# Kernel optimization log

Hardware: AMD Instinct MI355X
Metric: run time of the kernel (lower is better)

Reference implementation:

```python
import jax, jax.numpy as jnp
import numpy as np

N_ROW = 50000
N_COL = 50000
E = 600000
D = 128
NEG_SLOPE = 0.01  # torch LeakyReLU default


def _leaky(x):
    return jnp.where(x >= 0, x, NEG_SLOPE * x)


def _mlp(x, W1, b1, W2, b2):
    # (Linear -> LeakyReLU) x2, matching nn.Sequential in Conv_layer
    h = _leaky(x @ W1 + b1)
    return _leaky(h @ W2 + b2)


def setup_inputs() -> dict:
    key = jax.random.key(0)
    ks = jax.random.split(key, 16)
    inp = {
        "feat_row": jax.random.normal(ks[0], (N_ROW, D), jnp.float32),
        "feat_col": jax.random.normal(ks[1], (N_COL, D), jnp.float32),
        "src_c2r": jax.random.randint(ks[2], (E,), 0, N_COL, jnp.int32),
        "dst_c2r": jax.random.randint(ks[3], (E,), 0, N_ROW, jnp.int32),
        "w_c2r": jax.random.uniform(ks[4], (E,), jnp.float32),
        "src_r2c": jax.random.randint(ks[5], (E,), 0, N_ROW, jnp.int32),
        "dst_r2c": jax.random.randint(ks[6], (E,), 0, N_COL, jnp.int32),
        "w_r2c": jax.random.uniform(ks[7], (E,), jnp.float32),
        "W1_c2r": jax.random.normal(ks[8], (D, D), jnp.float32) / np.sqrt(D),
        "b1_c2r": jax.random.normal(ks[9], (D,), jnp.float32) * 0.01,
        "W2_c2r": jax.random.normal(ks[10], (D, D), jnp.float32) / np.sqrt(D),
        "b2_c2r": jax.random.normal(ks[11], (D,), jnp.float32) * 0.01,
        "W1_r2c": jax.random.normal(ks[12], (D, D), jnp.float32) / np.sqrt(D),
        "b1_r2c": jax.random.normal(ks[13], (D,), jnp.float32) * 0.01,
        "W2_r2c": jax.random.normal(ks[14], (D, D), jnp.float32) / np.sqrt(D),
        "b2_r2c": jax.random.normal(ks[15], (D,), jnp.float32) * 0.01,
        "eps_c2r": jnp.zeros((), jnp.float32),  # DGL GINConv init_eps=0
        "eps_r2c": jnp.zeros((), jnp.float32),
    }
    return inp


def reference(feat_row, feat_col, src_c2r, dst_c2r, w_c2r, src_r2c, dst_r2c, w_r2c,
              W1_c2r, b1_c2r, W2_c2r, b2_c2r, W1_r2c, b1_r2c, W2_r2c, b2_r2c,
              eps_c2r, eps_r2c):
    # col -> row GINConv (edge-weighted sum aggregation)
    msg = feat_col[src_c2r] * w_c2r[:, None]                       # [E, D]
    agg_row = jax.ops.segment_sum(msg, dst_c2r, num_segments=N_ROW)
    h_row = _mlp((1.0 + eps_c2r) * feat_row + agg_row, W1_c2r, b1_c2r, W2_c2r, b2_c2r)
    # row -> col GINConv using updated row features
    msg2 = h_row[src_r2c] * w_r2c[:, None]                         # [E, D]
    agg_col = jax.ops.segment_sum(msg2, dst_r2c, num_segments=N_COL)
    h_col = _mlp((1.0 + eps_r2c) * feat_col + agg_col, W1_r2c, b1_r2c, W2_r2c, b2_r2c)
    # residual (use_residual=True): add pre-conv embeddings
    return h_row + feat_row, h_col + feat_col
```

## Files before the change

kernel.cpp:

```cpp
#include <hip/hip_runtime.h>
#include <hip/hip_bf16.h>

#define NROW 50000
#define NCOL 50000
#define DDIM 128
#define CAP  32

typedef __bf16 bf16_t;
typedef __bf16 bf16x2 __attribute__((ext_vector_type(2)));
typedef __bf16 bf16x8 __attribute__((ext_vector_type(8)));
typedef float  f32x4  __attribute__((ext_vector_type(4)));

__device__ __forceinline__ float lrelu(float v) { return v >= 0.f ? v : 0.01f * v; }

__device__ __forceinline__ float ldf(const void* p, size_t i, bool f) {
    return f ? ((const float*)p)[i] : (float)((const bf16_t*)p)[i];
}

__device__ __forceinline__ bool dtf(const int* flags, int fi) {
    return (fi == -1) ? true : (fi == -2) ? false : (flags[fi] != 0);
}

struct TensorTab { const void* p[18]; int n[18]; };

__global__ __launch_bounds__(256) void detect_zero(TensorTab T, int* flags,
                                                   int* z, int zn)
{
    const int tid = threadIdx.x;
    if (blockIdx.x >= 18) {
        int i = (blockIdx.x - 18) * 256 + tid;
        if (i < zn) z[i] = 0;
        return;
    }
    __shared__ int vb, vf;
    const int t = blockIdx.x;
    if (tid == 0) { vb = 0; vf = 0; }
    __syncthreads();
    const int n = T.n[t];
    const bool isFloatArr = (t != 2 && t != 3 && t != 5 && t != 6) && n >= 2;
    if (isFloatArr) {
        int nw = n / 2;
        int wi = (int)(((long long)tid * nw) >> 8);
        unsigned w = ((const unsigned*)T.p[t])[wi];
        unsigned low = w & 0xffffu;
        if (low) {
            int e = (int)((low >> 7) & 0xffu);
            if (e >= 90 && e <= 141) atomicAdd(&vb, 1);
            else                     atomicAdd(&vf, 1);
        }
    }
    __syncthreads();
    if (tid == 0) flags[t] = (isFloatArr && vf > vb) ? 1 : 0;
}

__device__ __forceinline__ void fill_edges(
    int e, const int* __restrict__ dst, const int* __restrict__ srcArr,
    const void* __restrict__ wArr, int nE, int* __restrict__ counts,
    int2* __restrict__ slots2, int* __restrict__ ovCnt,
    int* __restrict__ ovList, bool fW)
{
    if (e >= nE) return;
    int d = dst[e];
    int pos = atomicAdd(&counts[d], 1);
    if (pos < CAP) {
        int2 pk;
        pk.x = srcArr[e];
        pk.y = __float_as_int(ldf(wArr, e, fW));
        slots2[(size_t)d * CAP + pos] = pk;
    } else {
        int k = atomicAdd(ovCnt, 1);
        ovList[k] = e;
    }
}

struct WPtrs { const void* W[4]; int fi[4]; };

__device__ __forceinline__ void prep_one(WPtrs P, const int* flags,
                                         __bf16* wfp, int slot)
{
    if (slot >= 4 * 2048) return;
    int m = slot >> 11, sIdx = slot & 2047;
    bool f = flags[P.fi[m]] != 0;
    int l = sIdx & 63, combo = sIdx >> 6;
    int ct = combo >> 2, kk = combo & 3;
    int col  = ct * 16 + (l & 15);
    int krow = kk * 32 + (l >> 4) * 8;
    bf16x8 v;
#pragma unroll
    for (int j = 0; j < 8; ++j)
        v[j] = (__bf16)ldf(P.W[m], (size_t)(krow + j) * DDIM + col, f);
    ((bf16x8*)wfp)[slot] = v;
}

__device__ __forceinline__ void convert_one(const void* __restrict__ feat,
                                            __bf16* __restrict__ cbuf,
                                            int i, int n8, bool f)
{
    if (i >= n8) return;
    bf16x8 v;
    if (f) {
        f32x4 a = ((const f32x4*)feat)[i * 2];
        f32x4 c = ((const f32x4*)feat)[i * 2 + 1];
#pragma unroll
        for (int j = 0; j < 4; ++j) { v[j] = (__bf16)a[j]; v[j + 4] = (__bf16)c[j]; }
    } else {
        v = ((const bf16x8*)feat)[i];
    }
    ((bf16x8*)cbuf)[i] = v;
}

__global__ __launch_bounds__(1024) void prep_fill_i2(
    WPtrs P, const int* __restrict__ flags, __bf16* __restrict__ wfp,
    const void* __restrict__ feat, __bf16* __restrict__ cbuf, int n8,
    int fiFeat, int cb, int eb, int K7,
    const int* __restrict__ f_dst, const int* __restrict__ f_src,
    const void* __restrict__ f_w, int f_nE, int* __restrict__ f_counts,
    int2* __restrict__ f_slots2, int* __restrict__ f_ovCnt,
    int* __restrict__ f_ovList, int f_fiW)
{
    const int g = blockIdx.x;
    const int tid = threadIdx.x;
    if (g >= K7) {
        prep_one(P, flags, wfp, (g - K7) * 1024 + tid);
        return;
    }
    int grp = g / 7, rem = g % 7;
    if (rem < 4) {
        int b = grp * 4 + rem;
        if (b >= cb) return;
        convert_one(feat, cbuf, b * 1024 + tid, n8, dtf(flags, fiFeat));
    } else {
        int b = grp * 3 + (rem - 4);
        if (b >= eb) return;
        fill_edges(b * 1024 + tid, f_dst, f_src, f_w, f_nE, f_counts,
                   f_slots2, f_ovCnt, f_ovList, dtf(flags, f_fiW));
    }
}

template <bool RESIDUAL, bool HOUT>
__global__ __launch_bounds__(1024) void mlp_fused2(
    const __bf16* __restrict__ gsrc, const int* __restrict__ counts,
    const int2* __restrict__ slots2, const int* __restrict__ srcArr,
    const int* __restrict__ dstArr, const void* __restrict__ wArr,
    const int* __restrict__ ovList, const int* __restrict__ ovCount, int fiW,
    const void* __restrict__ feat, const void* __restrict__ b1,
    const void* __restrict__ b2, const void* __restrict__ epsp,
    float* __restrict__ out, int N, const int* __restrict__ flags,
    int fiFeat, int fiB1, int fiB2, int fiEps,
    const __bf16* __restrict__ pW1, const __bf16* __restrict__ pW2,
    __bf16* __restrict__ hout,
    int mlpBlocks, int fillBlocks,
    const int* __restrict__ f_dst, const int* __restrict__ f_src,
    const void* __restrict__ f_w, int f_nE, int* __restrict__ f_counts,
    int2* __restrict__ f_slots2, int* __restrict__ f_ovCnt,
    int* __restrict__ f_ovList, int f_fiW)
{
    __shared__ alignas(16) __bf16 At[16 * 136];
    __shared__ alignas(16) __bf16 H1[16 * 136];

    const int tid = threadIdx.x;
    int bid;
    if (f_dst) {
        int grp = (int)blockIdx.x / 7, rem = (int)blockIdx.x % 7;
        if (rem >= 4) {
            int b = grp * 3 + (rem - 4);
            if (b < fillBlocks)
                fill_edges(b * 1024 + tid, f_dst, f_src, f_w, f_nE, f_counts,
                           f_slots2, f_ovCnt, f_ovList, dtf(flags, f_fiW));
            return;
        }
        bid = grp * 4 + rem;
        if (bid >= mlpBlocks) return;
    } else {
        bid = blockIdx.x;
        if (bid >= mlpBlocks) return;
    }

    const bool fF  = flags[fiFeat] != 0;
    const bool fB1 = flags[fiB1] != 0;
    const bool fB2 = flags[fiB2] != 0;
    const bool fE  = flags[fiEps] != 0;

    const int lane = tid & 63;
    const int wave = tid >> 6;
    const int quad = lane >> 4;
    const int r    = lane & 15;
    const int rowBase = bid * 16;
    const float eps1 = 1.f + ldf(epsp, 0, fE);

    {
        const bf16x2* fb = (const bf16x2*)gsrc;
        int row = rowBase + wave;
        bf16x2 o;
        if (row < N) {
            int cntRaw = counts[row];
            int cnt = cntRaw > CAP ? CAP : cntRaw;
            int sr = 0; float wv = 0.f;
            if (lane < cnt) {
                int2 pk = slots2[(size_t)row * CAP + lane];
                sr = pk.x;
                wv = __int_as_float(pk.y);
            }
            float2 acc0 = {0.f, 0.f}, acc1 = {0.f, 0.f};
            int i = 0;
            for (; i + 4 <= cnt; i += 4) {
                int   a0 = __shfl(sr, i),     a1 = __shfl(sr, i + 1);
                int   a2 = __shfl(sr, i + 2), a3 = __shfl(sr, i + 3);
                float w0 = __shfl(wv, i),     w1 = __shfl(wv, i + 1);
                float w2 = __shfl(wv, i + 2), w3 = __shfl(wv, i + 3);
                bf16x2 v0 = fb[(size_t)a0 * 64 + lane];
                bf16x2 v1 = fb[(size_t)a1 * 64 + lane];
                bf16x2 v2 = fb[(size_t)a2 * 64 + lane];
                bf16x2 v3 = fb[(size_t)a3 * 64 + lane];
                acc0.x += (float)v0[0] * w0; acc0.y += (float)v0[1] * w0;
                acc1.x += (float)v1[0] * w1; acc1.y += (float)v1[1] * w1;
                acc0.x += (float)v2[0] * w2; acc0.y += (float)v2[1] * w2;
                acc1.x += (float)v3[0] * w3; acc1.y += (float)v3[1] * w3;
            }
            for (; i < cnt; ++i) {
                int   a0 = __shfl(sr, i);
                float w0 = __shfl(wv, i);
                bf16x2 v0 = fb[(size_t)a0 * 64 + lane];
                acc0.x += (float)v0[0] * w0; acc0.y += (float)v0[1] * w0;
            }
            if (cntRaw > CAP) {
                const bool fW = dtf(flags, fiW);
                int nOv = *ovCount;
                for (int k = 0; k < nOv; ++k) {
                    int e = ovList[k];
                    if (dstArr[e] == row) {
                        int s = srcArr[e];
                        float wf = ldf(wArr, e, fW);
                        bf16x2 v = fb[(size_t)s * 64 + lane];
                        acc0.x += (float)v[0] * wf;
                        acc0.y += (float)v[1] * wf;
                    }
                }
            }
            float ax = acc0.x + acc1.x, ay = acc0.y + acc1.y;
            float f0, f1;
            if (fF) {
                float2 fv = ((const float2*)((const float*)feat +
                             (size_t)row * DDIM))[lane];
                f0 = fv.x; f1 = fv.y;
            } else {
                bf16x2 fv = ((const bf16x2*)((const bf16_t*)feat +
                             (size_t)row * DDIM))[lane];
                f0 = (float)fv[0]; f1 = (float)fv[1];
            }
            o[0] = (__bf16)(f0 * eps1 + ax);
            o[1] = (__bf16)(f1 * eps1 + ay);
        } else {
            o[0] = (__bf16)0.f; o[1] = (__bf16)0.f;
        }
        *(bf16x2*)&At[wave * 136 + lane * 2] = o;
    }
    __syncthreads();

    const int ct = wave;
    if (wave < 8) {
        bf16x8 a[4];
#pragma unroll
        for (int kk = 0; kk < 4; ++kk)
            a[kk] = *(const bf16x8*)&At[r * 136 + kk * 32 + quad * 8];
        const bf16x8* pw1v = (const bf16x8*)pW1;
        bf16x8 w1f[4];
#pragma unroll
        for (int kk = 0; kk < 4; ++kk)
            w1f[kk] = pw1v[(ct * 4 + kk) * 64 + lane];
        float b1v = ldf(b1, ct * 16 + r, fB1);
        f32x4 acc = {0.f, 0.f, 0.f, 0.f};
#pragma unroll
        for (int kk = 0; kk < 4; ++kk)
            acc = __builtin_amdgcn_mfma_f32_16x16x32_bf16(a[kk], w1f[kk], acc, 0, 0, 0);
#pragma unroll
        for (int gg = 0; gg < 4; ++gg)
            H1[(quad * 4 + gg) * 136 + ct * 16 + r] = (__bf16)lrelu(acc[gg] + b1v);
    }
    __syncthreads();

    if (wave < 8) {
        bf16x8 a2[4];
#pragma unroll
        for (int kk = 0; kk < 4; ++kk)
            a2[kk] = *(const bf16x8*)&H1[r * 136 + kk * 32 + quad * 8];
        const bf16x8* pw2v = (const bf16x8*)pW2;
        bf16x8 w2f[4];
#pragma unroll
        for (int kk = 0; kk < 4; ++kk)
            w2f[kk] = pw2v[(ct * 4 + kk) * 64 + lane];
        float b2v = ldf(b2, ct * 16 + r, fB2);
        f32x4 acc = {0.f, 0.f, 0.f, 0.f};
#pragma unroll
        for (int kk = 0; kk < 4; ++kk)
            acc = __builtin_amdgcn_mfma_f32_16x16x32_bf16(a2[kk], w2f[kk], acc, 0, 0, 0);
#pragma unroll
        for (int gg = 0; gg < 4; ++gg) {
            int row = rowBase + quad * 4 + gg;
            float v = lrelu(acc[gg] + b2v);
            if (HOUT)
                At[(quad * 4 + gg) * 136 + ct * 16 + r] = (__bf16)v;
            if (row < N) {
                int col = ct * 16 + r;
                if (RESIDUAL) v += ldf(feat, (size_t)row * DDIM + col, fF);
                out[(size_t)row * DDIM + col] = v;
            }
        }
    }

    if (HOUT) {
        __syncthreads();
        if (tid < 256) {
            int row = tid >> 4;
            int k0  = (tid & 15) * 8;
            int g   = rowBase + row;
            if (g < N)
                *(bf16x8*)&hout[(size_t)g * DDIM + k0] =
                    *(const bf16x8*)&At[row * 136 + k0];
        }
    }
}

__global__ __launch_bounds__(256) void prep_fill(
    WPtrs P, const int* __restrict__ flags, __bf16* __restrict__ wfp,
    const void* __restrict__ feat, __bf16* __restrict__ cbuf, int n8,
    int fiFeat, int cblocks,
    const int* __restrict__ f_dst, const int* __restrict__ f_src,
    const void* __restrict__ f_w, int f_nE, int* __restrict__ f_counts,
    int2* __restrict__ f_slots2, int* __restrict__ f_ovCnt,
    int* __restrict__ f_ovList, int f_fiW)
{
    const int b = blockIdx.x;
    const int tid = threadIdx.x;
    if (b < cblocks) {
        convert_one(feat, cbuf, b * 256 + tid, n8, dtf(flags, fiFeat));
    } else if (b < cblocks + 32) {
        prep_one(P, flags, wfp, (b - cblocks) * 256 + tid);
    } else {
        int e = (b - cblocks - 32) * 256 + tid;
        fill_edges(e, f_dst, f_src, f_w, f_nE, f_counts, f_slots2,
                   f_ovCnt, f_ovList, dtf(flags, f_fiW));
    }
}

__global__ __launch_bounds__(256) void segsum_scan(
    const __bf16* __restrict__ gsrc, const int* __restrict__ counts,
    const int2* __restrict__ slots2, float* __restrict__ agg, int nRows,
    const int* __restrict__ srcArr, const int* __restrict__ dstArr,
    const void* __restrict__ wArr, const int* __restrict__ ovList,
    const int* __restrict__ ovCount, const int* __restrict__ flags, int fiW)
{
    int row = blockIdx.x * 4 + (threadIdx.x >> 6);
    if (row >= nRows) return;
    int lane = threadIdx.x & 63;

    int cntRaw = counts[row];
    int cnt = cntRaw > CAP ? CAP : cntRaw;

    int sr = 0; float wv = 0.f;
    if (lane < cnt) {
        int2 pk = slots2[(size_t)row * CAP + lane];
        sr = pk.x;
        wv = __int_as_float(pk.y);
    }

    float2* ap = (float2*)(agg + (size_t)row * DDIM) + lane;
    float2 acc0 = {0.f, 0.f}, acc1 = {0.f, 0.f};

    const bf16x2* fb = (const bf16x2*)gsrc;
    int i = 0;
    for (; i + 4 <= cnt; i += 4) {
        int   a0 = __shfl(sr, i),     a1 = __shfl(sr, i + 1);
        int   a2 = __shfl(sr, i + 2), a3 = __shfl(sr, i + 3);
        float w0 = __shfl(wv, i),     w1 = __shfl(wv, i + 1);
        float w2 = __shfl(wv, i + 2), w3 = __shfl(wv, i + 3);
        bf16x2 v0 = fb[(size_t)a0 * 64 + lane];
        bf16x2 v1 = fb[(size_t)a1 * 64 + lane];
        bf16x2 v2 = fb[(size_t)a2 * 64 + lane];
        bf16x2 v3 = fb[(size_t)a3 * 64 + lane];
        acc0.x += (float)v0[0] * w0; acc0.y += (float)v0[1] * w0;
        acc1.x += (float)v1[0] * w1; acc1.y += (float)v1[1] * w1;
        acc0.x += (float)v2[0] * w2; acc0.y += (float)v2[1] * w2;
        acc1.x += (float)v3[0] * w3; acc1.y += (float)v3[1] * w3;
    }
    for (; i < cnt; ++i) {
        int   a0 = __shfl(sr, i);
        float w0 = __shfl(wv, i);
        bf16x2 v0 = fb[(size_t)a0 * 64 + lane];
        acc0.x += (float)v0[0] * w0; acc0.y += (float)v0[1] * w0;
    }
    if (cntRaw > CAP) {
        const bool fW = dtf(flags, fiW);
        int nOv = *ovCount;
        for (int k = 0; k < nOv; ++k) {
            int e = ovList[k];
            if (dstArr[e] == row) {
                int s = srcArr[e];
                float wf = ldf(wArr, e, fW);
                bf16x2 v = fb[(size_t)s * 64 + lane];
                acc0.x += (float)v[0] * wf; acc0.y += (float)v[1] * wf;
            }
        }
    }
    acc0.x += acc1.x; acc0.y += acc1.y;
    *ap = acc0;
}

template <bool RESIDUAL, bool HOUT>
__global__ __launch_bounds__(256) void mlp_cs(
    const void* __restrict__ feat, const float* __restrict__ agg,
    const void* __restrict__ b1, const void* __restrict__ b2,
    const void* __restrict__ epsp, float* __restrict__ out, int N,
    const int* __restrict__ flags, int fiFeat, int fiB1, int fiB2, int fiEps,
    const __bf16* __restrict__ pW1, const __bf16* __restrict__ pW2,
    __bf16* __restrict__ hout,
    int mblocks,
    const int* __restrict__ f_dst, const int* __restrict__ f_src,
    const void* __restrict__ f_w, int f_nE, int* __restrict__ f_counts,
    int2* __restrict__ f_slots2, int* __restrict__ f_ovCnt,
    int* __restrict__ f_ovList, int f_fiW)
{
    __shared__ alignas(16) __bf16 At[16 * 136];
    __shared__ alignas(16) __bf16 H1[16 * 136];

    const int tid = threadIdx.x;
    if (f_dst && (int)blockIdx.x >= mblocks) {
        int e = ((int)blockIdx.x - mblocks) * 256 + tid;
        fill_edges(e, f_dst, f_src, f_w, f_nE, f_counts, f_slots2,
                   f_ovCnt, f_ovList, dtf(flags, f_fiW));
        return;
    }

    const bool fF  = flags[fiFeat] != 0;
    const bool fB1 = flags[fiB1] != 0;
    const bool fB2 = flags[fiB2] != 0;
    const bool fE  = flags[fiEps] != 0;

    const int lane = tid & 63;
    const int wave = tid >> 6;
    const int quad = lane >> 4;
    const int r    = lane & 15;
    const int rowBase = blockIdx.x * 16;
    const float eps1 = 1.f + ldf(epsp, 0, fE);

    {
        int row = tid >> 4;
        int k0  = (tid & 15) * 8;
        int g   = rowBase + row;
        bf16x8 av;
        if (g < N) {
            size_t base = (size_t)g * DDIM + k0;
            const f32x4* gp = (const f32x4*)(agg + base);
            f32x4 g0 = gp[0], g1 = gp[1];
            if (fF) {
                const f32x4* fp = (const f32x4*)((const float*)feat + base);
                f32x4 f0 = fp[0], f1 = fp[1];
#pragma unroll
                for (int j = 0; j < 4; ++j) {
                    av[j]     = (__bf16)(f0[j] * eps1 + g0[j]);
                    av[j + 4] = (__bf16)(f1[j] * eps1 + g1[j]);
                }
            } else {
                bf16x8 fv = *(const bf16x8*)((const bf16_t*)feat + base);
#pragma unroll
                for (int j = 0; j < 4; ++j) {
                    av[j]     = (__bf16)((float)fv[j]     * eps1 + g0[j]);
                    av[j + 4] = (__bf16)((float)fv[j + 4] * eps1 + g1[j]);
                }
            }
        } else {
#pragma unroll
            for (int j = 0; j < 8; ++j) av[j] = (__bf16)0.f;
        }
        *(bf16x8*)&At[row * 136 + k0] = av;
    }
    __syncthreads();

    bf16x8 a[4];
#pragma unroll
    for (int kk = 0; kk < 4; ++kk)
        a[kk] = *(const bf16x8*)&At[r * 136 + kk * 32 + quad * 8];

    const int ct0 = wave * 2, ct1 = ct0 + 1;

    const bf16x8* pw1v = (const bf16x8*)pW1;
    bf16x8 wfa[4], wfb[4];
#pragma unroll
    for (int kk = 0; kk < 4; ++kk) {
        wfa[kk] = pw1v[(ct0 * 4 + kk) * 64 + lane];
        wfb[kk] = pw1v[(ct1 * 4 + kk) * 64 + lane];
    }
    float b1a = ldf(b1, ct0 * 16 + r, fB1);
    float b1b = ldf(b1, ct1 * 16 + r, fB1);

    {
        f32x4 acc = {0.f, 0.f, 0.f, 0.f};
#pragma unroll
        for (int kk = 0; kk < 4; ++kk)
            acc = __builtin_amdgcn_mfma_f32_16x16x32_bf16(a[kk], wfa[kk], acc, 0, 0, 0);
#pragma unroll
        for (int gg = 0; gg < 4; ++gg)
            H1[(quad * 4 + gg) * 136 + ct0 * 16 + r] = (__bf16)lrelu(acc[gg] + b1a);
    }
    {
        f32x4 acc = {0.f, 0.f, 0.f, 0.f};
#pragma unroll
        for (int kk = 0; kk < 4; ++kk)
            acc = __builtin_amdgcn_mfma_f32_16x16x32_bf16(a[kk], wfb[kk], acc, 0, 0, 0);
#pragma unroll
        for (int gg = 0; gg < 4; ++gg)
            H1[(quad * 4 + gg) * 136 + ct1 * 16 + r] = (__bf16)lrelu(acc[gg] + b1b);
    }
    __syncthreads();

    bf16x8 a2[4];
#pragma unroll
    for (int kk = 0; kk < 4; ++kk)
        a2[kk] = *(const bf16x8*)&H1[r * 136 + kk * 32 + quad * 8];

    const bf16x8* pw2v = (const bf16x8*)pW2;
#pragma unroll
    for (int kk = 0; kk < 4; ++kk) {
        wfa[kk] = pw2v[(ct0 * 4 + kk) * 64 + lane];
        wfb[kk] = pw2v[(ct1 * 4 + kk) * 64 + lane];
    }
    float b2a = ldf(b2, ct0 * 16 + r, fB2);
    float b2b = ldf(b2, ct1 * 16 + r, fB2);

#pragma unroll
    for (int cp = 0; cp < 2; ++cp) {
        const int ct = cp ? ct1 : ct0;
        f32x4 acc = {0.f, 0.f, 0.f, 0.f};
#pragma unroll
        for (int kk = 0; kk < 4; ++kk)
            acc = __builtin_amdgcn_mfma_f32_16x16x32_bf16(
                a2[kk], cp ? wfb[kk] : wfa[kk], acc, 0, 0, 0);
        float bias = cp ? b2b : b2a;
#pragma unroll
        for (int gg = 0; gg < 4; ++gg) {
            int row = rowBase + quad * 4 + gg;
            float v = lrelu(acc[gg] + bias);
            if (HOUT)
                At[(quad * 4 + gg) * 136 + ct * 16 + r] = (__bf16)v;
            if (row < N) {
                int col = ct * 16 + r;
                if (RESIDUAL) v += ldf(feat, (size_t)row * DDIM + col, fF);
                out[(size_t)row * DDIM + col] = v;
            }
        }
    }

    if (HOUT) {
        __syncthreads();
        int row = tid >> 4;
        int k0  = (tid & 15) * 8;
        int g   = rowBase + row;
        if (g < N)
            *(bf16x8*)&hout[(size_t)g * DDIM + k0] =
                *(const bf16x8*)&At[row * 136 + k0];
    }
}

__global__ __launch_bounds__(256) void scatter_any(
    const void* __restrict__ feat, const int* __restrict__ src,
    const int* __restrict__ dst, const void* __restrict__ w,
    float* __restrict__ agg, int nE,
    const int* __restrict__ flags, int fiFeat, int fiW)
{
    const bool fF = dtf(flags, fiFeat);
    const bool fW = dtf(flags, fiW);
    int g = blockIdx.x * 256 + threadIdx.x;
    int e = g >> 5;
    if (e >= nE) return;
    int c = (g & 31) << 2;
    int s = src[e], d = dst[e];
    float wf = ldf(w, e, fW);
    size_t base = (size_t)s * DDIM + c;
    float* ap = agg + (size_t)d * DDIM + c;
    unsafeAtomicAdd(ap + 0, ldf(feat, base + 0, fF) * wf);
    unsafeAtomicAdd(ap + 1, ldf(feat, base + 1, fF) * wf);
    unsafeAtomicAdd(ap + 2, ldf(feat, base + 2, fF) * wf);
    unsafeAtomicAdd(ap + 3, ldf(feat, base + 3, fF) * wf);
}

__global__ __launch_bounds__(256) void residual_add(
    float* __restrict__ out, const void* __restrict__ feat, int n4,
    const int* __restrict__ flags, int fiFeat)
{
    const bool fF = flags[fiFeat] != 0;
    int i = blockIdx.x * 256 + threadIdx.x;
    if (i >= n4) return;
    f32x4 o = ((const f32x4*)out)[i];
    f32x4 r;
#pragma unroll
    for (int j = 0; j < 4; ++j) r[j] = o[j] + ldf(feat, (size_t)i * 4 + j, fF);
    ((f32x4*)out)[i] = r;
}

__device__ __forceinline__ void fill_wfrag(const void* __restrict__ W, bool f,
                                           __bf16* wf, int tid)
{
#pragma unroll
    for (int i = 0; i < 8; ++i) {
        int sIdx  = tid + i * 256;
        int l     = sIdx & 63;
        int combo = sIdx >> 6;
        int ct = combo >> 2, kk = combo & 3;
        int col  = ct * 16 + (l & 15);
        int krow = kk * 32 + (l >> 4) * 8;
        __bf16* dp = wf + (size_t)sIdx * 8;
#pragma unroll
        for (int j = 0; j < 8; ++j)
            dp[j] = (__bf16)ldf(W, (size_t)(krow + j) * DDIM + col, f);
    }
}

template <bool RESIDUAL>
__global__ __launch_bounds__(256) void mlp_kernel(
    const void* __restrict__ feat, const float* __restrict__ agg,
    const void* __restrict__ W1, const void* __restrict__ b1,
    const void* __restrict__ W2, const void* __restrict__ b2,
    const void* __restrict__ epsp, float* __restrict__ out, int N,
    const int* __restrict__ flags,
    int fiFeat, int fiW1, int fiB1, int fiW2, int fiB2, int fiEps)
{
    __shared__ alignas(16) __bf16 wf[32 * 64 * 8];
    __shared__ alignas(16) __bf16 h1t[64 * 136];

    const bool fF  = flags[fiFeat] != 0;
    const bool fB1 = flags[fiB1] != 0;
    const bool fB2 = flags[fiB2] != 0;
    const bool fE  = flags[fiEps] != 0;

    const int tid  = threadIdx.x;
    const int lane = tid & 63;
    const int wave = tid >> 6;
    const int quad = lane >> 4;
    const int r    = lane & 15;

    fill_wfrag(W1, flags[fiW1] != 0, wf, tid);

    const float eps1 = 1.f + ldf(epsp, 0, fE);
    const int rowBase = blockIdx.x * 64 + wave * 16;

    bf16x8 a[4];
    {
        int rowA = rowBase + r;
        if (rowA < N) {
            size_t fb = (size_t)rowA * DDIM + quad * 8;
            const f32x4* gp = (const f32x4*)(agg + fb);
            if (fF) {
                const f32x4* fp = (const f32x4*)((const float*)feat + fb);
#pragma unroll
                for (int kk = 0; kk < 4; ++kk) {
                    f32x4 f0 = fp[kk * 8], f1 = fp[kk * 8 + 1];
                    f32x4 g0 = gp[kk * 8], g1 = gp[kk * 8 + 1];
                    bf16x8 av;
#pragma unroll
                    for (int j = 0; j < 4; ++j) {
                        av[j]     = (__bf16)(f0[j] * eps1 + g0[j]);
                        av[j + 4] = (__bf16)(f1[j] * eps1 + g1[j]);
                    }
                    a[kk] = av;
                }
            } else {
                const bf16x8* fp = (const bf16x8*)((const bf16_t*)feat + fb);
#pragma unroll
                for (int kk = 0; kk < 4; ++kk) {
                    bf16x8 fv = fp[kk * 4];
                    f32x4 g0 = gp[kk * 8], g1 = gp[kk * 8 + 1];
                    bf16x8 av;
#pragma unroll
                    for (int j = 0; j < 4; ++j) {
                        av[j]     = (__bf16)((float)fv[j]     * eps1 + g0[j]);
                        av[j + 4] = (__bf16)((float)fv[j + 4] * eps1 + g1[j]);
                    }
                    a[kk] = av;
                }
            }
        } else {
#pragma unroll
            for (int kk = 0; kk < 4; ++kk)
#pragma unroll
                for (int j = 0; j < 8; ++j) a[kk][j] = (__bf16)0.f;
        }
    }

    __syncthreads();

    const bf16x8* wv = (const bf16x8*)wf;
#pragma unroll
    for (int ct = 0; ct < 8; ++ct) {
        f32x4 acc = {0.f, 0.f, 0.f, 0.f};
#pragma unroll
        for (int kk = 0; kk < 4; ++kk)
            acc = __builtin_amdgcn_mfma_f32_16x16x32_bf16(
                a[kk], wv[(ct * 4 + kk) * 64 + lane], acc, 0, 0, 0);
        float bias = ldf(b1, ct * 16 + r, fB1);
#pragma unroll
        for (int gg = 0; gg < 4; ++gg)
            h1t[(wave * 16 + quad * 4 + gg) * 136 + ct * 16 + r] =
                (__bf16)lrelu(acc[gg] + bias);
    }
    __syncthreads();

    bf16x8 a2[4];
#pragma unroll
    for (int kk = 0; kk < 4; ++kk)
        a2[kk] = *(const bf16x8*)&h1t[(wave * 16 + r) * 136 + kk * 32 + quad * 8];

    fill_wfrag(W2, flags[fiW2] != 0, wf, tid);
    __syncthreads();

#pragma unroll
    for (int ct = 0; ct < 8; ++ct) {
        f32x4 acc = {0.f, 0.f, 0.f, 0.f};
#pragma unroll
        for (int kk = 0; kk < 4; ++kk)
            acc = __builtin_amdgcn_mfma_f32_16x16x32_bf16(
                a2[kk], wv[(ct * 4 + kk) * 64 + lane], acc, 0, 0, 0);
        float bias = ldf(b2, ct * 16 + r, fB2);
#pragma unroll
        for (int gg = 0; gg < 4; ++gg) {
            int row = rowBase + quad * 4 + gg;
            if (row < N) {
                int col = ct * 16 + r;
                float v = lrelu(acc[gg] + bias);
                if (RESIDUAL) v += ldf(feat, (size_t)row * DDIM + col, fF);
                out[(size_t)row * DDIM + col] = v;
            }
        }
    }
}

extern "C" void kernel_launch(void* const* d_in, const int* in_sizes, int n_in,
                              void* d_out, int out_size, void* d_ws, size_t ws_size,
                              hipStream_t stream)
{
    const int* src_c2r = (const int*)d_in[2];
    const int* dst_c2r = (const int*)d_in[3];
    const int* src_r2c = (const int*)d_in[5];
    const int* dst_r2c = (const int*)d_in[6];
    const int nE = in_sizes[2];

    char* wsb = (char*)d_ws;
    int*    flags  = (int*)wsb;
    __bf16* wfprep = (__bf16*)(wsb + 128);

    int*    cntA   = (int*)(wsb + 128 + 131072);
    int*    ovCntA = cntA + NROW;
    int*    cntB   = cntA + NROW + 8;
    int*    ovCntB = cntA + 2 * NROW + 8;
    size_t  o5 = 128 + 131072 + ((size_t)2 * NROW + 16) * 4;
    o5 = (o5 + 15) & ~(size_t)15;
    int2*   sl2A = (int2*)(wsb + o5);  o5 += (size_t)NROW * CAP * 8;
    int2*   sl2B = (int2*)(wsb + o5);  o5 += (size_t)NROW * CAP * 8;
    int*    ovLA = (int*)(wsb + o5);   o5 += (size_t)nE * 4;
    int*    ovLB = (int*)(wsb + o5);   o5 += (size_t)nE * 4;
    o5 = (o5 + 15) & ~(size_t)15;
    __bf16* cbX  = (__bf16*)(wsb + o5); o5 += (size_t)NCOL * DDIM * 2;
    __bf16* cbH  = (__bf16*)(wsb + o5); o5 += (size_t)NROW * DDIM * 2;
    const size_t NEED_A5 = o5;

    size_t  ofsA2   = 128 + 131072 + ((size_t)2 * NROW + 16) * 4;
    ofsA2 = (ofsA2 + 15) & ~(size_t)15;
    int2*   slots2A2  = (int2*)(wsb + ofsA2);
    size_t  ofsOvA2   = ofsA2 + (size_t)NROW * CAP * 8;
    int*    ovListA2  = (int*)(wsb + ofsOvA2);
    int*    ovListB2  = ovListA2 + nE;
    size_t  ofsCbA2   = (ofsOvA2 + (size_t)nE * 8 + 15) & ~(size_t)15;
    __bf16* cbufA2    = (__bf16*)(wsb + ofsCbA2);
    const size_t NEED_A2 = ofsCbA2 + (size_t)NROW * DDIM * 2;

    const bool tierA5 = ws_size >= NEED_A5;
    const bool tierA2 = ws_size >= NEED_A2;

    TensorTab T;
    for (int i = 0; i < 18; ++i) { T.p[i] = d_in[i]; T.n[i] = in_sizes[i]; }

    float* out_row = (float*)d_out;
    float* out_col = out_row + (size_t)NROW * DDIM;
    const size_t aggBytes = (size_t)NROW * DDIM * sizeof(float);

    const int eblocks  = (nE + 255) / 256;
    const int sblocks  = (nE * 32 + 255) / 256;
    const int mblocksR = (NROW + 63) / 64;
    const int mblocksC = (NCOL + 63) / 64;
    const int csR      = (NROW + 15) / 16;
    const int csC      = (NCOL + 15) / 16;
    const int gblocksR = (NROW + 3) / 4;
    const int gblocksC = (NCOL + 3) / 4;
    const int cblocks  = (NCOL * DDIM / 8 + 255) / 256;
    const int zn2      = 2 * NROW + 16;
    const int zb2      = (zn2 + 255) / 256;

    WPtrs P;
    P.W[0] = d_in[8];  P.fi[0] = 8;
    P.W[1] = d_in[10]; P.fi[1] = 10;
    P.W[2] = d_in[12]; P.fi[2] = 12;
    P.W[3] = d_in[14]; P.fi[3] = 14;

    if (tierA5) {
        const int n8  = NCOL * DDIM / 8;
        const int cb4 = (n8 + 1023) / 1024;
        const int eb4 = (nE + 1023) / 1024;
        detect_zero<<<18 + zb2, 256, 0, stream>>>(T, flags, cntA, zn2);
        {
            int ka = (cb4 + 3) / 4, kb = (eb4 + 2) / 3;
            int K = ka > kb ? ka : kb;
            prep_fill_i2<<<7 * K + 8, 1024, 0, stream>>>(
                P, flags, wfprep, d_in[1], cbX, n8, 1, cb4, eb4, 7 * K,
                dst_c2r, src_c2r, d_in[4], nE, cntA, sl2A, ovCntA, ovLA, 4);
        }
        {
            int ka = (csR + 3) / 4, kb = (eb4 + 2) / 3;
            int K = ka > kb ? ka : kb;
            mlp_fused2<true, true><<<7 * K, 1024, 0, stream>>>(
                cbX, cntA, sl2A, src_c2r, dst_c2r, d_in[4], ovLA, ovCntA, 4,
                d_in[0], d_in[9], d_in[11], d_in[16],
                out_row, NROW, flags, 0, 9, 11, 16,
                wfprep + 0 * 16384, wfprep + 1 * 16384, cbH,
                csR, eb4, dst_r2c, src_r2c, d_in[7], nE, cntB, sl2B,
                ovCntB, ovLB, 7);
        }
        mlp_fused2<true, false><<<csC, 1024, 0, stream>>>(
            cbH, cntB, sl2B, src_r2c, dst_r2c, d_in[7], ovLB, ovCntB, 7,
            d_in[1], d_in[13], d_in[15], d_in[17],
            out_col, NCOL, flags, 1, 13, 15, 17,
            wfprep + 2 * 16384, wfprep + 3 * 16384, nullptr,
            csC, 0, nullptr, nullptr, nullptr, 0, nullptr, nullptr,
            nullptr, nullptr, 0);
    } else if (tierA2) {
        detect_zero<<<18 + zb2, 256, 0, stream>>>(T, flags, cntA, zn2);
        prep_fill<<<cblocks + 32 + eblocks, 256, 0, stream>>>(
            P, flags, wfprep, d_in[1], cbufA2, NCOL * DDIM / 8, 1, cblocks,
            dst_c2r, src_c2r, d_in[4], nE, cntA, slots2A2, ovCntA,
            ovListA2, 4);
        segsum_scan<<<gblocksR, 256, 0, stream>>>(cbufA2, cntA, slots2A2,
            out_col, NROW, src_c2r, dst_c2r, d_in[4], ovListA2, ovCntA,
            flags, 4);
        mlp_cs<true, true><<<csR + eblocks, 256, 0, stream>>>(
            d_in[0], out_col, d_in[9], d_in[11], d_in[16],
            out_row, NROW, flags, 0, 9, 11, 16,
            wfprep + 0 * 16384, wfprep + 1 * 16384, cbufA2,
            csR, dst_r2c, src_r2c, d_in[7], nE, cntB, slots2A2,
            ovCntB, ovListB2, 7);
        segsum_scan<<<gblocksC, 256, 0, stream>>>(cbufA2, cntB, slots2A2,
            out_col, NCOL, src_r2c, dst_r2c, d_in[7], ovListB2, ovCntB,
            flags, 7);
        mlp_cs<true, false><<<csC, 256, 0, stream>>>(
            d_in[1], out_col, d_in[13], d_in[15], d_in[17],
            out_col, NCOL, flags, 1, 13, 15, 17,
            wfprep + 2 * 16384, wfprep + 3 * 16384, nullptr,
            csC, nullptr, nullptr, nullptr, 0, nullptr, nullptr,
            nullptr, nullptr, 0);
    } else {
        detect_zero<<<18, 256, 0, stream>>>(T, flags, nullptr, 0);
        hipMemsetAsync(out_col, 0, aggBytes, stream);
        scatter_any<<<sblocks, 256, 0, stream>>>(d_in[1], src_c2r, dst_c2r,
            d_in[4], out_col, nE, flags, 1, 4);
        mlp_kernel<false><<<mblocksR, 256, 0, stream>>>(
            d_in[0], out_col, d_in[8], d_in[9], d_in[10], d_in[11], d_in[16],
            out_row, NROW, flags, 0, 8, 9, 10, 11, 16);

        hipMemsetAsync(out_col, 0, aggBytes, stream);
        scatter_any<<<sblocks, 256, 0, stream>>>(out_row, src_r2c, dst_r2c,
            d_in[7], out_col, nE, flags, -1, 7);
        residual_add<<<(NROW * DDIM / 4 + 255) / 256, 256, 0, stream>>>(
            out_row, d_in[0], NROW * DDIM / 4, flags, 0);
        mlp_kernel<true><<<mblocksC, 256, 0, stream>>>(
            d_in[1], out_col, d_in[12], d_in[13], d_in[14], d_in[15], d_in[17],
            out_col, NCOL, flags, 1, 12, 13, 14, 15, 17);
    }
}
```

Measured before the change: 306.2 us.

## Split fused gather+MLP into separate segsum and MLP kernels with interleaved fill

Replaces the 1024-thread fused kernel, which gathered neighbour features and ran the two-layer MFMA MLP in one block, with a 256-thread segment-sum kernel that writes an fp32 aggregate, followed by the existing mlp_cs kernel. The second-direction edge-slot fill still runs interleaved in the first segsum launch. The aim is better occupancy and latency hiding for the gather, since in the fused version most waves sat idle during the MLP phase. The cost is an extra round trip of the fp32 aggregate buffer through global memory and two more kernel launches.

```diff
diff --git a/kernel.cpp b/kernel.cpp
--- a/kernel.cpp
+++ b/kernel.cpp
@@ -137,27 +137,18 @@
     }
 }
 
-template <bool RESIDUAL, bool HOUT>
-__global__ __launch_bounds__(1024) void mlp_fused2(
+__global__ __launch_bounds__(256) void segsum_fill_i(
     const __bf16* __restrict__ gsrc, const int* __restrict__ counts,
-    const int2* __restrict__ slots2, const int* __restrict__ srcArr,
-    const int* __restrict__ dstArr, const void* __restrict__ wArr,
-    const int* __restrict__ ovList, const int* __restrict__ ovCount, int fiW,
-    const void* __restrict__ feat, const void* __restrict__ b1,
-    const void* __restrict__ b2, const void* __restrict__ epsp,
-    float* __restrict__ out, int N, const int* __restrict__ flags,
-    int fiFeat, int fiB1, int fiB2, int fiEps,
-    const __bf16* __restrict__ pW1, const __bf16* __restrict__ pW2,
-    __bf16* __restrict__ hout,
-    int mlpBlocks, int fillBlocks,
+    const int2* __restrict__ slots2, float* __restrict__ agg, int nRows,
+    const int* __restrict__ srcArr, const int* __restrict__ dstArr,
+    const void* __restrict__ wArr, const int* __restrict__ ovList,
+    const int* __restrict__ ovCount, const int* __restrict__ flags, int fiW,
+    int segBlocks, int fillBlocks,
     const int* __restrict__ f_dst, const int* __restrict__ f_src,
     const void* __restrict__ f_w, int f_nE, int* __restrict__ f_counts,
     int2* __restrict__ f_slots2, int* __restrict__ f_ovCnt,
     int* __restrict__ f_ovList, int f_fiW)
 {
-    __shared__ alignas(16) __bf16 At[16 * 136];
-    __shared__ alignas(16) __bf16 H1[16 * 136];
-
     const int tid = threadIdx.x;
     int bid;
     if (f_dst) {
@@ -165,194 +156,20 @@
         if (rem >= 4) {
             int b = grp * 3 + (rem - 4);
             if (b < fillBlocks)
-                fill_edges(b * 1024 + tid, f_dst, f_src, f_w, f_nE, f_counts,
+                fill_edges(b * 256 + tid, f_dst, f_src, f_w, f_nE, f_counts,
                            f_slots2, f_ovCnt, f_ovList, dtf(flags, f_fiW));
             return;
         }
         bid = grp * 4 + rem;
-        if (bid >= mlpBlocks) return;
+        if (bid >= segBlocks) return;
     } else {
         bid = blockIdx.x;
-        if (bid >= mlpBlocks) return;
-    }
-
-    const bool fF  = flags[fiFeat] != 0;
-    const bool fB1 = flags[fiB1] != 0;
-    const bool fB2 = flags[fiB2] != 0;
-    const bool fE  = flags[fiEps] != 0;
-
-    const int lane = tid & 63;
-    const int wave = tid >> 6;
-    const int quad = lane >> 4;
-    const int r    = lane & 15;
-    const int rowBase = bid * 16;
-    const float eps1 = 1.f + ldf(epsp, 0, fE);
-
-    {
-        const bf16x2* fb = (const bf16x2*)gsrc;
-        int row = rowBase + wave;
-        bf16x2 o;
-        if (row < N) {
-            int cntRaw = counts[row];
-            int cnt = cntRaw > CAP ? CAP : cntRaw;
-            int sr = 0; float wv = 0.f;
-            if (lane < cnt) {
-                int2 pk = slots2[(size_t)row * CAP + lane];
-                sr = pk.x;
-                wv = __int_as_float(pk.y);
-            }
-            float2 acc0 = {0.f, 0.f}, acc1 = {0.f, 0.f};
-            int i = 0;
-            for (; i + 4 <= cnt; i += 4) {
-                int   a0 = __shfl(sr, i),     a1 = __shfl(sr, i + 1);
-                int   a2 = __shfl(sr, i + 2), a3 = __shfl(sr, i + 3);
-                float w0 = __shfl(wv, i),     w1 = __shfl(wv, i + 1);
-                float w2 = __shfl(wv, i + 2), w3 = __shfl(wv, i + 3);
-                bf16x2 v0 = fb[(size_t)a0 * 64 + lane];
-                bf16x2 v1 = fb[(size_t)a1 * 64 + lane];
-                bf16x2 v2 = fb[(size_t)a2 * 64 + lane];
-                bf16x2 v3 = fb[(size_t)a3 * 64 + lane];
-                acc0.x += (float)v0[0] * w0; acc0.y += (float)v0[1] * w0;
-                acc1.x += (float)v1[0] * w1; acc1.y += (float)v1[1] * w1;
-                acc0.x += (float)v2[0] * w2; acc0.y += (float)v2[1] * w2;
-                acc1.x += (float)v3[0] * w3; acc1.y += (float)v3[1] * w3;
-            }
-            for (; i < cnt; ++i) {
-                int   a0 = __shfl(sr, i);
-                float w0 = __shfl(wv, i);
-                bf16x2 v0 = fb[(size_t)a0 * 64 + lane];
-                acc0.x += (float)v0[0] * w0; acc0.y += (float)v0[1] * w0;
-            }
-            if (cntRaw > CAP) {
-                const bool fW = dtf(flags, fiW);
-                int nOv = *ovCount;
-                for (int k = 0; k < nOv; ++k) {
-                    int e = ovList[k];
-                    if (dstArr[e] == row) {
-                        int s = srcArr[e];
-                        float wf = ldf(wArr, e, fW);
-                        bf16x2 v = fb[(size_t)s * 64 + lane];
-                        acc0.x += (float)v[0] * wf;
-                        acc0.y += (float)v[1] * wf;
-                    }
-                }
-            }
-            float ax = acc0.x + acc1.x, ay = acc0.y + acc1.y;
-            float f0, f1;
-            if (fF) {
-                float2 fv = ((const float2*)((const float*)feat +
-                             (size_t)row * DDIM))[lane];
-                f0 = fv.x; f1 = fv.y;
-            } else {
-                bf16x2 fv = ((const bf16x2*)((const bf16_t*)feat +
-                             (size_t)row * DDIM))[lane];
-                f0 = (float)fv[0]; f1 = (float)fv[1];
-            }
-            o[0] = (__bf16)(f0 * eps1 + ax);
-            o[1] = (__bf16)(f1 * eps1 + ay);
-        } else {
-            o[0] = (__bf16)0.f; o[1] = (__bf16)0.f;
-        }
-        *(bf16x2*)&At[wave * 136 + lane * 2] = o;
-    }
-    __syncthreads();
-
-    const int ct = wave;
-    if (wave < 8) {
-        bf16x8 a[4];
-#pragma unroll
-        for (int kk = 0; kk < 4; ++kk)
-            a[kk] = *(const bf16x8*)&At[r * 136 + kk * 32 + quad * 8];
-        const bf16x8* pw1v = (const bf16x8*)pW1;
-        bf16x8 w1f[4];
-#pragma unroll
-        for (int kk = 0; kk < 4; ++kk)
-            w1f[kk] = pw1v[(ct * 4 + kk) * 64 + lane];
-        float b1v = ldf(b1, ct * 16 + r, fB1);
-        f32x4 acc = {0.f, 0.f, 0.f, 0.f};
-#pragma unroll
-        for (int kk = 0; kk < 4; ++kk)
-            acc = __builtin_amdgcn_mfma_f32_16x16x32_bf16(a[kk], w1f[kk], acc, 0, 0, 0);
-#pragma unroll
-        for (int gg = 0; gg < 4; ++gg)
-            H1[(quad * 4 + gg) * 136 + ct * 16 + r] = (__bf16)lrelu(acc[gg] + b1v);
-    }
-    __syncthreads();
-
-    if (wave < 8) {
-        bf16x8 a2[4];
-#pragma unroll
-        for (int kk = 0; kk < 4; ++kk)
-            a2[kk] = *(const bf16x8*)&H1[r * 136 + kk * 32 + quad * 8];
-        const bf16x8* pw2v = (const bf16x8*)pW2;
-        bf16x8 w2f[4];
-#pragma unroll
-        for (int kk = 0; kk < 4; ++kk)
-            w2f[kk] = pw2v[(ct * 4 + kk) * 64 + lane];
-        float b2v = ldf(b2, ct * 16 + r, fB2);
-        f32x4 acc = {0.f, 0.f, 0.f, 0.f};
-#pragma unroll
-        for (int kk = 0; kk < 4; ++kk)
-            acc = __builtin_amdgcn_mfma_f32_16x16x32_bf16(a2[kk], w2f[kk], acc, 0, 0, 0);
-#pragma unroll
-        for (int gg = 0; gg < 4; ++gg) {
-            int row = rowBase + quad * 4 + gg;
-            float v = lrelu(acc[gg] + b2v);
-            if (HOUT)
-                At[(quad * 4 + gg) * 136 + ct * 16 + r] = (__bf16)v;
-            if (row < N) {
-                int col = ct * 16 + r;
-                if (RESIDUAL) v += ldf(feat, (size_t)row * DDIM + col, fF);
-                out[(size_t)row * DDIM + col] = v;
-            }
-        }
-    }
-
-    if (HOUT) {
-        __syncthreads();
-        if (tid < 256) {
-            int row = tid >> 4;
-            int k0  = (tid & 15) * 8;
-            int g   = rowBase + row;
-            if (g < N)
-                *(bf16x8*)&hout[(size_t)g * DDIM + k0] =
-                    *(const bf16x8*)&At[row * 136 + k0];
-        }
-    }
-}
-
-__global__ __launch_bounds__(256) void prep_fill(
-    WPtrs P, const int* __restrict__ flags, __bf16* __restrict__ wfp,
-    const void* __restrict__ feat, __bf16* __restrict__ cbuf, int n8,
-    int fiFeat, int cblocks,
-    const int* __restrict__ f_dst, const int* __restrict__ f_src,
-    const void* __restrict__ f_w, int f_nE, int* __restrict__ f_counts,
-    int2* __restrict__ f_slots2, int* __restrict__ f_ovCnt,
-    int* __restrict__ f_ovList, int f_fiW)
-{
-    const int b = blockIdx.x;
-    const int tid = threadIdx.x;
-    if (b < cblocks) {
-        convert_one(feat, cbuf, b * 256 + tid, n8, dtf(flags, fiFeat));
-    } else if (b < cblocks + 32) {
-        prep_one(P, flags, wfp, (b - cblocks) * 256 + tid);
-    } else {
-        int e = (b - cblocks - 32) * 256 + tid;
-        fill_edges(e, f_dst, f_src, f_w, f_nE, f_counts, f_slots2,
-                   f_ovCnt, f_ovList, dtf(flags, f_fiW));
-    }
-}
-
-__global__ __launch_bounds__(256) void segsum_scan(
-    const __bf16* __restrict__ gsrc, const int* __restrict__ counts,
-    const int2* __restrict__ slots2, float* __restrict__ agg, int nRows,
-    const int* __restrict__ srcArr, const int* __restrict__ dstArr,
-    const void* __restrict__ wArr, const int* __restrict__ ovList,
-    const int* __restrict__ ovCount, const int* __restrict__ flags, int fiW)
-{
-    int row = blockIdx.x * 4 + (threadIdx.x >> 6);
+        if (bid >= segBlocks) return;
+    }
+
+    int row = bid * 4 + (tid >> 6);
     if (row >= nRows) return;
-    int lane = threadIdx.x & 63;
+    int lane = tid & 63;
 
     int cntRaw = counts[row];
     int cnt = cntRaw > CAP ? CAP : cntRaw;
@@ -561,6 +378,28 @@
     }
 }
 
+__global__ __launch_bounds__(256) void prep_fill(
+    WPtrs P, const int* __restrict__ flags, __bf16* __restrict__ wfp,
+    const void* __restrict__ feat, __bf16* __restrict__ cbuf, int n8,
+    int fiFeat, int cblocks,
+    const int* __restrict__ f_dst, const int* __restrict__ f_src,
+    const void* __restrict__ f_w, int f_nE, int* __restrict__ f_counts,
+    int2* __restrict__ f_slots2, int* __restrict__ f_ovCnt,
+    int* __restrict__ f_ovList, int f_fiW)
+{
+    const int b = blockIdx.x;
+    const int tid = threadIdx.x;
+    if (b < cblocks) {
+        convert_one(feat, cbuf, b * 256 + tid, n8, dtf(flags, fiFeat));
+    } else if (b < cblocks + 32) {
+        prep_one(P, flags, wfp, (b - cblocks) * 256 + tid);
+    } else {
+        int e = (b - cblocks - 32) * 256 + tid;
+        fill_edges(e, f_dst, f_src, f_w, f_nE, f_counts, f_slots2,
+                   f_ovCnt, f_ovList, dtf(flags, f_fiW));
+    }
+}
+
 __global__ __launch_bounds__(256) void scatter_any(
     const void* __restrict__ feat, const int* __restrict__ src,
     const int* __restrict__ dst, const void* __restrict__ w,
@@ -760,7 +599,7 @@
     o5 = (o5 + 15) & ~(size_t)15;
     __bf16* cbX  = (__bf16*)(wsb + o5); o5 += (size_t)NCOL * DDIM * 2;
     __bf16* cbH  = (__bf16*)(wsb + o5); o5 += (size_t)NROW * DDIM * 2;
-    const size_t NEED_A5 = o5;
+    const size_t NEED_A8 = o5;
 
     size_t  ofsA2   = 128 + 131072 + ((size_t)2 * NROW + 16) * 4;
     ofsA2 = (ofsA2 + 15) & ~(size_t)15;
@@ -772,7 +611,7 @@
     __bf16* cbufA2    = (__bf16*)(wsb + ofsCbA2);
     const size_t NEED_A2 = ofsCbA2 + (size_t)NROW * DDIM * 2;
 
-    const bool tierA5 = ws_size >= NEED_A5;
+    const bool tierA8 = ws_size >= NEED_A8;
     const bool tierA2 = ws_size >= NEED_A2;
 
     TensorTab T;
@@ -800,7 +639,7 @@
     P.W[2] = d_in[12]; P.fi[2] = 12;
     P.W[3] = d_in[14]; P.fi[3] = 14;
 
-    if (tierA5) {
+    if (tierA8) {
         const int n8  = NCOL * DDIM / 8;
         const int cb4 = (n8 + 1023) / 1024;
         const int eb4 = (nE + 1023) / 1024;
@@ -813,22 +652,30 @@
                 dst_c2r, src_c2r, d_in[4], nE, cntA, sl2A, ovCntA, ovLA, 4);
         }
         {
-            int ka = (csR + 3) / 4, kb = (eb4 + 2) / 3;
+            int ka = (gblocksR + 3) / 4, kb = (eblocks + 2) / 3;
             int K = ka > kb ? ka : kb;
-            mlp_fused2<true, true><<<7 * K, 1024, 0, stream>>>(
-                cbX, cntA, sl2A, src_c2r, dst_c2r, d_in[4], ovLA, ovCntA, 4,
-                d_in[0], d_in[9], d_in[11], d_in[16],
-                out_row, NROW, flags, 0, 9, 11, 16,
-                wfprep + 0 * 16384, wfprep + 1 * 16384, cbH,
-                csR, eb4, dst_r2c, src_r2c, d_in[7], nE, cntB, sl2B,
-                ovCntB, ovLB, 7);
-        }
-        mlp_fused2<true, false><<<csC, 1024, 0, stream>>>(
-            cbH, cntB, sl2B, src_r2c, dst_r2c, d_in[7], ovLB, ovCntB, 7,
-            d_in[1], d_in[13], d_in[15], d_in[17],
+            segsum_fill_i<<<7 * K, 256, 0, stream>>>(
+                cbX, cntA, sl2A, out_col, NROW, src_c2r, dst_c2r, d_in[4],
+                ovLA, ovCntA, flags, 4,
+                gblocksR, eblocks, dst_r2c, src_r2c, d_in[7], nE, cntB,
+                sl2B, ovCntB, ovLB, 7);
+        }
+        mlp_cs<true, true><<<csR, 256, 0, stream>>>(
+            d_in[0], out_col, d_in[9], d_in[11], d_in[16],
+            out_row, NROW, flags, 0, 9, 11, 16,
+            wfprep + 0 * 16384, wfprep + 1 * 16384, cbH,
+            csR, nullptr, nullptr, nullptr, 0, nullptr, nullptr,
+            nullptr, nullptr, 0);
+        segsum_fill_i<<<gblocksC, 256, 0, stream>>>(
+            cbH, cntB, sl2B, out_col, NCOL, src_r2c, dst_r2c, d_in[7],
+            ovLB, ovCntB, flags, 7,
+            gblocksC, 0, nullptr, nullptr, nullptr, 0, nullptr,
+            nullptr, nullptr, nullptr, 0);
+        mlp_cs<true, false><<<csC, 256, 0, stream>>>(
+            d_in[1], out_col, d_in[13], d_in[15], d_in[17],
             out_col, NCOL, flags, 1, 13, 15, 17,
             wfprep + 2 * 16384, wfprep + 3 * 16384, nullptr,
-            csC, 0, nullptr, nullptr, nullptr, 0, nullptr, nullptr,
+            csC, nullptr, nullptr, nullptr, 0, nullptr, nullptr,
             nullptr, nullptr, 0);
     } else if (tierA2) {
         detect_zero<<<18 + zb2, 256, 0, stream>>>(T, flags, cntA, zn2);
@@ -836,18 +683,22 @@
             P, flags, wfprep, d_in[1], cbufA2, NCOL * DDIM / 8, 1, cblocks,
             dst_c2r, src_c2r, d_in[4], nE, cntA, slots2A2, ovCntA,
             ovListA2, 4);
-        segsum_scan<<<gblocksR, 256, 0, stream>>>(cbufA2, cntA, slots2A2,
-            out_col, NROW, src_c2r, dst_c2r, d_in[4], ovListA2, ovCntA,
-            flags, 4);
+        segsum_fill_i<<<gblocksR, 256, 0, stream>>>(
+            cbufA2, cntA, slots2A2, out_col, NROW, src_c2r, dst_c2r,
+            d_in[4], ovListA2, ovCntA, flags, 4,
+            gblocksR, 0, nullptr, nullptr, nullptr, 0, nullptr,
+            nullptr, nullptr, nullptr, 0);
         mlp_cs<true, true><<<csR + eblocks, 256, 0, stream>>>(
             d_in[0], out_col, d_in[9], d_in[11], d_in[16],
             out_row, NROW, flags, 0, 9, 11, 16,
             wfprep + 0 * 16384, wfprep + 1 * 16384, cbufA2,
             csR, dst_r2c, src_r2c, d_in[7], nE, cntB, slots2A2,
             ovCntB, ovListB2, 7);
-        segsum_scan<<<gblocksC, 256, 0, stream>>>(cbufA2, cntB, slots2A2,
-            out_col, NCOL, src_r2c, dst_r2c, d_in[7], ovListB2, ovCntB,
-            flags, 7);
+        segsum_fill_i<<<gblocksC, 256, 0, stream>>>(
+            cbufA2, cntB, slots2A2, out_col, NCOL, src_r2c, dst_r2c,
+            d_in[7], ovListB2, ovCntB, flags, 7,
+            gblocksC, 0, nullptr, nullptr, nullptr, 0, nullptr,
+            nullptr, nullptr, nullptr, 0);
         mlp_cs<true, false><<<csC, 256, 0, stream>>>(
             d_in[1], out_col, d_in[13], d_in[15], d_in[17],
             out_col, NCOL, flags, 1, 13, 15, 17,
```

After: 299.9 us. 1.02x faster.
